# Optimization experiments

Measured on AMD Instinct MI355X. Metric: run time of the kernel, lower is better.

## Reference

```python
import jax, jax.numpy as jnp
import numpy as np

C = 0.01      # ball curvature
SC = 0.1      # sqrt(c)
K = 20        # neighbors
EPS = 1e-15


def _norm(v):
    return jnp.sqrt(jnp.clip(jnp.sum(v * v, -1, keepdims=True), EPS))


def expmap0(u):
    n = _norm(u)
    return jnp.tanh(SC * n) * u / (SC * n)


def logmap0(x):
    n = _norm(x)
    t = jnp.clip(SC * n, 0.0, 1.0 - 1e-7)
    return jnp.arctanh(t) * x / (SC * n)


def mobius_add(x, y):
    x2 = jnp.sum(x * x, -1, keepdims=True)
    y2 = jnp.sum(y * y, -1, keepdims=True)
    xy = jnp.sum(x * y, -1, keepdims=True)
    num = (1 + 2 * C * xy + C * y2) * x + (1 - C * x2) * y
    den = 1 + 2 * C * xy + C * C * x2 * y2
    return num / jnp.clip(den, EPS)


def knn(x, k):
    # x: (B,N,C) -> (B,N,k) indices of nearest neighbors (largest -dist^2)
    xx = jnp.sum(x * x, -1)                                 # (B,N)
    pd = 2.0 * jnp.einsum('bnc,bmc->bnm', x, x) - xx[:, :, None] - xx[:, None, :]
    return jax.lax.top_k(pd, k)[1]


def gather(x, idx):
    # x: (B,N,C), idx: (B,N,k) -> (B,N,k,C)
    return jax.vmap(lambda xt, ix: xt[ix])(x, idx)


def batchnorm(y, g, b, axes):
    mu = jnp.mean(y, axes)
    var = jnp.var(y, axes)
    return (y - mu) / jnp.sqrt(var + 1e-5) * g + b


def edge_block(x, w, g, b):
    # x: (B,N,C) -> (B,N,Cout); 1x1 conv over concat(nbr - ctr, ctr)
    idx = knn(x, K)
    nb = gather(x, idx)                                     # (B,N,K,C)
    ctr = jnp.broadcast_to(x[:, :, None, :], nb.shape)
    f = jnp.concatenate([nb - ctr, ctr], -1)                # (B,N,K,2C)
    y = jnp.einsum('bnkc,oc->bnko', f, w)
    y = jax.nn.leaky_relu(batchnorm(y, g, b, (0, 1, 2)), 0.2)
    return jnp.max(y, axis=2)


def setup_inputs():
    key = jax.random.key(0)
    ks = jax.random.split(key, 6)
    B, N = 8, 1024
    return {
        'x': jax.random.normal(ks[0], (B, 3, N), jnp.float32),
        'W1': jax.random.normal(ks[1], (64, 6), jnp.float32) * 0.1,
        'w2': jax.random.normal(ks[2], (64, 128), jnp.float32) * 0.05,
        'g2': jnp.ones((64,), jnp.float32), 'b2': jnp.zeros((64,), jnp.float32),
        'w3': jax.random.normal(ks[3], (128, 128), jnp.float32) * 0.05,
        'g3': jnp.ones((128,), jnp.float32), 'b3': jnp.zeros((128,), jnp.float32),
        'w4': jax.random.normal(ks[4], (256, 256), jnp.float32) * 0.05,
        'g4': jnp.ones((256,), jnp.float32), 'b4': jnp.zeros((256,), jnp.float32),
        'w5': jax.random.normal(ks[5], (1024, 512), jnp.float32) * 0.05,
        'g5': jnp.ones((1024,), jnp.float32), 'b5': jnp.zeros((1024,), jnp.float32),
    }


def reference(x, W1, w2, g2, b2, w3, g3, b3, w4, g4, b4, w5, g5, b5):
    xt = jnp.transpose(x, (0, 2, 1))                        # (B,N,3)
    # --- hyperbolic edge features ---
    idx = knn(xt, K)                                        # knn in euclidean coords
    xp = expmap0(xt)                                        # ToPoincare
    nb = gather(xp, idx)                                    # (B,N,K,3)
    ctr = jnp.broadcast_to(xp[:, :, None, :], nb.shape)
    h = jnp.concatenate([mobius_add(nb, -ctr), ctr], -1)    # (B,N,K,6)
    # MobiusConv2d (kernel 1) == mobius matvec: expmap0(W @ logmap0(x))
    h = expmap0(logmap0(h) @ W1.T)                          # (B,N,K,64)
    # MobiusBatchNorm2d (tangent-space normalization, bias=False)
    u = logmap0(h)
    mu = jnp.mean(u, axis=(0, 1, 2))
    uc = u - mu
    var = jnp.mean(jnp.sum(uc * uc, -1))
    h = expmap0(uc / jnp.sqrt(var + 1e-5))
    # Radial LeakyReLU in tangent space
    h = expmap0(jax.nn.leaky_relu(logmap0(h), 0.2))
    x1 = logmap0(jnp.max(h, axis=2))                        # max over k, FromPoincare -> (B,N,64)
    # --- euclidean DGCNN stack ---
    x2 = edge_block(x1, w2, g2, b2)                         # (B,N,64)
    x3 = edge_block(x2, w3, g3, b3)                         # (B,N,128)
    x4 = edge_block(x3, w4, g4, b4)                         # (B,N,256)
    feat = jnp.concatenate([x1, x2, x3, x4], -1)            # (B,N,512)
    y = jnp.einsum('bnc,oc->bno', feat, w5)                 # (B,N,1024)
    y = jax.nn.leaky_relu(batchnorm(y, g5, b5, (0, 1)), 0.2)
    return jnp.max(y, axis=1)                               # (B,1024)
```

## Files before the change

### kernel.cpp

```cpp
#include <hip/hip_runtime.h>
#include <math.h>

#define KNN 20
constexpr int B_ = 8, N_ = 1024, BN_ = B_ * N_;
constexpr int NEDGE = BN_ * KNN;

using f32x4 = __attribute__((ext_vector_type(4))) float;
using s8v = __attribute__((ext_vector_type(8))) short;
typedef unsigned long long u64;

__device__ __forceinline__ float wave_sum(float v) {
#pragma unroll
  for (int off = 32; off >= 1; off >>= 1) v += __shfl_xor(v, off, 64);
  return v;
}

__device__ __forceinline__ unsigned sortable(float f) {
  unsigned u = __float_as_uint(f);
  return u ^ ((u & 0x80000000u) ? 0xFFFFFFFFu : 0x80000000u);
}

__device__ __forceinline__ unsigned short rne_bf16(float f) {
  unsigned u = __float_as_uint(f);
  unsigned r = (u + 0x7FFFu + ((u >> 16) & 1u)) >> 16;
  return (unsigned short)r;
}

__device__ __forceinline__ u64 packkey(float v, int m) {
  return ((u64)sortable(v) << 10) | (u64)(1023 - m);
}

__device__ __forceinline__ void sort16_desc(u64 (&v)[16]) {
#pragma unroll
  for (int p = 1; p < 16; p <<= 1)
#pragma unroll
    for (int k = p; k >= 1; k >>= 1)
#pragma unroll
      for (int j = k & (p - 1); j + k < 16; j += 2 * k)
#pragma unroll
        for (int i = 0; i < k && i + j + k < 16; ++i)
          if ((i + j) / (2 * p) == (i + j + k) / (2 * p)) {
            u64 a = v[i + j], b = v[i + j + k];
            bool sw = a < b;
            v[i + j] = sw ? b : a;
            v[i + j + k] = sw ? a : b;
          }
}

__device__ __forceinline__ u64 bitonic64_desc(u64 B, int lane) {
#pragma unroll
  for (int k = 2; k <= 64; k <<= 1)
#pragma unroll
    for (int j = k >> 1; j > 0; j >>= 1) {
      u64 o = __shfl_xor(B, j, 64);
      bool up = ((lane & k) != 0);
      bool lower = ((lane & j) == 0);
      bool keepMin = (up == lower);
      bool takeOther = keepMin ? (o < B) : (o > B);
      B = takeOther ? o : B;
    }
  return B;
}

__device__ __forceinline__ void topk20_sorted(u64 (&v)[16], int lane,
                                              int* __restrict__ outp) {
  sort16_desc(v);
  u64 B = v[0];
#pragma unroll
  for (int s = 0; s < 15; ++s) v[s] = v[s + 1];
  v[15] = 0;
  B = bitonic64_desc(B, lane);
  for (int sel = 0; sel < KNN; ++sel) {
    u64 win = __shfl(B, 0, 64);
    int m = 1023 - (int)(win & 1023ull);
    if (lane == 0) outp[sel] = m;
    int origin = m & 63;
    u64 ins = __shfl(v[0], origin, 64);
    bool isorig = (lane == origin);
#pragma unroll
    for (int s = 0; s < 15; ++s) v[s] = isorig ? v[s + 1] : v[s];
    v[15] = isorig ? 0 : v[15];
    u64 Bs = __shfl_down(B, 1, 64);
    if (lane == 63) Bs = 0;
    unsigned long long ball = __ballot(Bs > ins);
    int pos = __popcll(ball);
    u64 Bup = __shfl_up(Bs, 1, 64);
    B = (lane < pos) ? Bs : (lane == pos ? ins : Bup);
  }
}

__global__ void k_prep(const float* __restrict__ x, float* __restrict__ xp) {
  int i = blockIdx.x * 256 + threadIdx.x;
  int b = i >> 10, n = i & 1023;
  float v0 = x[(b * 3 + 0) * N_ + n];
  float v1 = x[(b * 3 + 1) * N_ + n];
  float v2 = x[(b * 3 + 2) * N_ + n];
  float nsq = v0 * v0 + v1 * v1 + v2 * v2;
  float nn = sqrtf(fmaxf(nsq, 1e-15f));
  float s = tanhf(0.1f * nn) / (0.1f * nn);
  xp[i * 3 + 0] = s * v0; xp[i * 3 + 1] = s * v1; xp[i * 3 + 2] = s * v2;
}

__global__ __launch_bounds__(256) void k_knn3s(const float* __restrict__ x,
                                               int* __restrict__ idx) {
  __shared__ float4 pts4[N_];
  int t = threadIdx.x;
  int row0 = blockIdx.x * 4;
  int b = row0 >> 10;
  const float* xb = x + (size_t)b * 3 * N_;
  for (int i = t; i < N_; i += 256) {
    float px = xb[i], py = xb[N_ + i], pz = xb[2 * N_ + i];
    pts4[i] = make_float4(px, py, pz, px * px + py * py + pz * pz);
  }
  __syncthreads();
  int lane = t & 63, w = t >> 6;
  int row = row0 + w, rl = row & 1023;
  float4 c = pts4[rl];
  u64 v[16];
#pragma unroll
  for (int s = 0; s < 16; ++s) {
    int m = lane + 64 * s;
    float4 q = pts4[m];
    float dot = c.x * q.x + c.y * q.y + c.z * q.z;
    float val = 2.f * dot - c.w - q.w;
    v[s] = packkey(val, m);
  }
  topk20_sorted(v, lane, idx + (size_t)row * KNN);
}

__global__ __launch_bounds__(256) void k_topks(const float* __restrict__ pd,
                                               int* __restrict__ idx) {
  int t = threadIdx.x, lane = t & 63, w = t >> 6;
  int row = blockIdx.x * 4 + w;
  const float* rp = pd + (size_t)row * N_;
  u64 v[16];
#pragma unroll
  for (int s = 0; s < 16; ++s) v[s] = packkey(rp[lane + 64 * s], lane + 64 * s);
  topk20_sorted(v, lane, idx + (size_t)row * KNN);
}

__global__ __launch_bounds__(256) void k_hgeom(const float* __restrict__ xp,
                                               const int* __restrict__ idx,
                                               float* __restrict__ fgeo,
                                               float* __restrict__ mom) {
  int e = blockIdx.x * 256 + threadIdx.x;
  int gw = e / KNN;
  int b = gw >> 10;
  int nbr = idx[e];
  const float* pc = xp + (size_t)gw * 3;
  float c0 = pc[0], c1 = pc[1], c2 = pc[2];
  const float* pn = xp + ((size_t)(b << 10) + nbr) * 3;
  float a0 = pn[0], a1 = pn[1], a2 = pn[2];
  float x2 = a0 * a0 + a1 * a1 + a2 * a2;
  float y2 = c0 * c0 + c1 * c1 + c2 * c2;
  float xy = -(a0 * c0 + a1 * c1 + a2 * c2);
  float f1 = 1.f + 0.02f * xy + 0.01f * y2;
  float f2 = 1.f - 0.01f * x2;
  float den = 1.f + 0.02f * xy + 0.0001f * x2 * y2;
  float rden = 1.f / fmaxf(den, 1e-15f);
  float m0 = (f1 * a0 - f2 * c0) * rden;
  float m1 = (f1 * a1 - f2 * c1) * rden;
  float m2 = (f1 * a2 - f2 * c2) * rden;
  float nsq = m0 * m0 + m1 * m1 + m2 * m2 + y2;
  float nn = sqrtf(fmaxf(nsq, 1e-15f));
  float sn = 0.1f * nn;
  float tt = fminf(sn, 1.f - 1e-7f);
  float s = atanhf(tt) / sn;
  float f[6] = {s * m0, s * m1, s * m2, s * c0, s * c1, s * c2};
#pragma unroll
  for (int j = 0; j < 6; ++j) fgeo[j * NEDGE + e] = f[j];
  float mm[27];
  {
    int q = 0;
#pragma unroll
    for (int i = 0; i < 6; ++i) mm[q++] = f[i];
#pragma unroll
    for (int i = 0; i < 6; ++i)
#pragma unroll
      for (int j = i; j < 6; ++j) mm[q++] = f[i] * f[j];
  }
#pragma unroll
  for (int m = 0; m < 27; ++m) mm[m] = wave_sum(mm[m]);
  __shared__ float part[4][27];
  int lane = threadIdx.x & 63, w = threadIdx.x >> 6;
  if (lane == 0) {
#pragma unroll
    for (int m = 0; m < 27; ++m) part[w][m] = mm[m];
  }
  __syncthreads();
  int t = threadIdx.x;
  if (t < 27) {
    float v = part[0][t] + part[1][t] + part[2][t] + part[3][t];
    atomicAdd(&mom[t * 16 + (blockIdx.x & 15)], v);
  }
}

__global__ void k_hfin2(const float* __restrict__ mom,
                        const float* __restrict__ w1, float* mu64,
                        float* invv) {
  __shared__ float M[27];
  int t = threadIdx.x;
  if (t < 27) {
    float s = 0.f;
    for (int k = 0; k < 16; ++k) s += mom[t * 16 + k];
    M[t] = s * (1.f / (float)NEDGE);
  }
  __syncthreads();
  float w1r[6];
#pragma unroll
  for (int j = 0; j < 6; ++j) w1r[j] = w1[t * 6 + j];
  float mu = 0.f;
#pragma unroll
  for (int j = 0; j < 6; ++j) mu = fmaf(w1r[j], M[j], mu);
  float q = 0.f;
  {
    int off = 6;
#pragma unroll
    for (int i = 0; i < 6; ++i) {
      q = fmaf(w1r[i] * w1r[i], M[off], q); ++off;
#pragma unroll
      for (int j = i + 1; j < 6; ++j) {
        q = fmaf(2.f * w1r[i] * w1r[j], M[off], q); ++off;
      }
    }
  }
  float varc = q - mu * mu;
  float var = wave_sum(varc);
  mu64[t] = mu;
  if (t == 0) invv[0] = 1.f / sqrtf(var + 1e-5f);
}

__global__ __launch_bounds__(256) void k_hyper_x1(
    const float* __restrict__ fgeo, const float* __restrict__ w1,
    const float* __restrict__ mu64, const float* __restrict__ invv,
    float* __restrict__ x1, float* __restrict__ xx,
    unsigned short* __restrict__ fb) {
  int t = threadIdx.x, lane = t & 63, w = t >> 6;
  int gw = blockIdx.x * 4 + w;
  float w1r[6];
#pragma unroll
  for (int j = 0; j < 6; ++j) w1r[j] = w1[lane * 6 + j];
  float f[6] = {0.f, 0.f, 0.f, 0.f, 0.f, 0.f};
  if (lane < KNN) {
    int e = gw * KNN + lane;
#pragma unroll
    for (int j = 0; j < 6; ++j) f[j] = fgeo[j * NEDGE + e];
  }
  float mu = mu64[lane];
  float inv = invv[0];
  float mx = -INFINITY;
  for (int k = 0; k < KNN; ++k) {
    float u = 0.f;
#pragma unroll
    for (int j = 0; j < 6; ++j) u = fmaf(w1r[j], __shfl(f[j], k), u);
    float vv = (u - mu) * inv;
    float l = vv > 0.f ? vv : 0.2f * vv;
    float nsq = wave_sum(l * l);
    float nn = sqrtf(fmaxf(nsq, 1e-15f));
    float sn = 0.1f * nn;
    float sc = tanhf(sn) / sn;
    mx = fmaxf(mx, sc * l);
  }
  float msq = wave_sum(mx * mx);
  float mn = sqrtf(fmaxf(msq, 1e-15f));
  float sn = 0.1f * mn;
  float tt = fminf(sn, 1.f - 1e-7f);
  float val = atanhf(tt) / sn * mx;
  x1[(size_t)gw * 64 + lane] = val;
  fb[(size_t)gw * 512 + lane] = rne_bf16(val);
  float xs = wave_sum(val * val);
  if (lane == 0) xx[gw] = xs;
}

__device__ __forceinline__ void load_t68(float (&Lt)[64][68],
                                         const float* __restrict__ src,
                                         int ldr, int t) {
  int row = t >> 2, kq = (t & 3) * 16;
  const float* p = src + (size_t)row * ldr + kq;
  float4 v0 = *(const float4*)(p);
  float4 v1 = *(const float4*)(p + 4);
  float4 v2 = *(const float4*)(p + 8);
  float4 v3 = *(const float4*)(p + 12);
  Lt[kq + 0][row] = v0.x;  Lt[kq + 1][row] = v0.y;
  Lt[kq + 2][row] = v0.z;  Lt[kq + 3][row] = v0.w;
  Lt[kq + 4][row] = v1.x;  Lt[kq + 5][row] = v1.y;
  Lt[kq + 6][row] = v1.z;  Lt[kq + 7][row] = v1.w;
  Lt[kq + 8][row] = v2.x;  Lt[kq + 9][row] = v2.y;
  Lt[kq + 10][row] = v2.z; Lt[kq + 11][row] = v2.w;
  Lt[kq + 12][row] = v3.x; Lt[kq + 13][row] = v3.y;
  Lt[kq + 14][row] = v3.z; Lt[kq + 15][row] = v3.w;
}

template <int CIN>
__global__ __launch_bounds__(256) void k_pd2(const float* __restrict__ xin,
                                             const float* __restrict__ xx,
                                             float* __restrict__ pd) {
  __shared__ float At[64][68], Bt[64][68];
  int b = blockIdx.z;
  int n0 = blockIdx.x * 64, m0 = blockIdx.y * 64;
  int t = threadIdx.x;
  int tr4 = (t >> 4) * 4, tc4 = (t & 15) * 4;
  float acc[4][4] = {};
  const float* xb = xin + (size_t)b * N_ * CIN;
  for (int c0 = 0; c0 < CIN; c0 += 64) {
    if (c0) __syncthreads();
    load_t68(At, xb + (size_t)n0 * CIN + c0, CIN, t);
    load_t68(Bt, xb + (size_t)m0 * CIN + c0, CIN, t);
    __syncthreads();
#pragma unroll 4
    for (int k = 0; k < 64; ++k) {
      float4 a = *(const float4*)&At[k][tr4];
      float4 bb = *(const float4*)&Bt[k][tc4];
      float av[4] = {a.x, a.y, a.z, a.w};
      float bv[4] = {bb.x, bb.y, bb.z, bb.w};
#pragma unroll
      for (int ii = 0; ii < 4; ++ii)
#pragma unroll
        for (int jj = 0; jj < 4; ++jj) acc[ii][jj] = fmaf(av[ii], bv[jj], acc[ii][jj]);
    }
  }
  const float* xxn = xx + b * N_;
#pragma unroll
  for (int ii = 0; ii < 4; ++ii) {
    int r = n0 + tr4 + ii;
#pragma unroll
    for (int jj = 0; jj < 4; ++jj) {
      int c = m0 + tc4 + jj;
      pd[((size_t)b * N_ + r) * N_ + c] = 2.f * acc[ii][jj] - xxn[r] - xxn[c];
    }
  }
}

template <int CIN, int COUT>
__global__ __launch_bounds__(256) void k_xw2(const float* __restrict__ xin,
                                             const float* __restrict__ w,
                                             float* __restrict__ Y,
                                             float* __restrict__ Z) {
  __shared__ float At[64][68], Bt[64][68];
  int n0 = blockIdx.x * 64;
  int j0 = blockIdx.y * 64;
  float* outp; int obase, coff;
  if (j0 < COUT) { outp = Y; obase = j0; coff = 0; }
  else { outp = Z; obase = j0 - COUT; coff = CIN; }
  int t = threadIdx.x;
  int tr4 = (t >> 4) * 4, tc4 = (t & 15) * 4;
  float acc[4][4] = {};
  for (int c0 = 0; c0 < CIN; c0 += 64) {
    if (c0) __syncthreads();
    load_t68(At, xin + (size_t)n0 * CIN + c0, CIN, t);
    load_t68(Bt, w + (size_t)obase * (2 * CIN) + coff + c0, 2 * CIN, t);
    __syncthreads();
#pragma unroll 4
    for (int k = 0; k < 64; ++k) {
      float4 a = *(const float4*)&At[k][tr4];
      float4 bb = *(const float4*)&Bt[k][tc4];
      float av[4] = {a.x, a.y, a.z, a.w};
      float bv[4] = {bb.x, bb.y, bb.z, bb.w};
#pragma unroll
      for (int ii = 0; ii < 4; ++ii)
#pragma unroll
        for (int jj = 0; jj < 4; ++jj) acc[ii][jj] = fmaf(av[ii], bv[jj], acc[ii][jj]);
    }
  }
#pragma unroll
  for (int ii = 0; ii < 4; ++ii)
#pragma unroll
    for (int jj = 0; jj < 4; ++jj)
      outp[(size_t)(n0 + tr4 + ii) * COUT + obase + tc4 + jj] = acc[ii][jj];
}

template <int COUT>
__global__ __launch_bounds__(256) void k_gather2(
    const float* __restrict__ Y, const float* __restrict__ Z,
    const int* __restrict__ idx, float* gsum, float* gsq,
    float* __restrict__ xout) {
  constexpr int J = COUT / 64;
  int t = threadIdx.x, lane = t & 63, w = t >> 6;
  int bn = blockIdx.x * 4 + w;
  int b = bn >> 10;
  int myidx = 0;
  if (lane < KNN) myidx = idx[(size_t)bn * KNN + lane];
  float base[J], acc[J], acc2[J], mx[J];
#pragma unroll
  for (int j = 0; j < J; ++j) {
    int o = lane + 64 * j;
    base[j] = Z[(size_t)bn * COUT + o] - Y[(size_t)bn * COUT + o];
    acc[j] = 0.f; acc2[j] = 0.f; mx[j] = -INFINITY;
  }
  for (int k = 0; k < KNN; ++k) {
    int nbr = __shfl(myidx, k);
    const float* yr = Y + ((size_t)(b << 10) + nbr) * COUT;
#pragma unroll
    for (int j = 0; j < J; ++j) {
      float v = yr[lane + 64 * j] + base[j];
      acc[j] += v; acc2[j] += v * v; mx[j] = fmaxf(mx[j], v);
    }
  }
  int bkt = bn & 31;
#pragma unroll
  for (int j = 0; j < J; ++j) {
    atomicAdd(&gsum[bkt * 1024 + lane + 64 * j], acc[j]);
    atomicAdd(&gsq[bkt * 1024 + lane + 64 * j], acc2[j]);
    xout[(size_t)bn * COUT + lane + 64 * j] = mx[j];
  }
}

template <int COUT, bool WXX, bool WOUT>
__global__ void k_apply(float* __restrict__ xio,
                        const float* __restrict__ aArr,
                        const float* __restrict__ cArr,
                        unsigned short* __restrict__ fb, int coloff,
                        float* __restrict__ xx) {
  constexpr int J = COUT / 64;
  int t = threadIdx.x, lane = t & 63, w = t >> 6;
  int bn = blockIdx.x * 4 + w;
  float s = 0.f;
#pragma unroll
  for (int j = 0; j < J; ++j) {
    int o = lane + 64 * j;
    float v = xio[(size_t)bn * COUT + o];
    float u = aArr[o] * v + cArr[o];
    u = u > 0.f ? u : 0.2f * u;
    if (WOUT) xio[(size_t)bn * COUT + o] = u;
    fb[(size_t)bn * 512 + coloff + o] = rne_bf16(u);
    if (WXX) s = fmaf(u, u, s);
  }
  if (WXX) {
    s = wave_sum(s);
    if (lane == 0) xx[bn] = s;
  }
}

__global__ void k_bnfin(const float* gsum, const float* gsq,
                        const float* __restrict__ g, const float* __restrict__ bb,
                        float* aArr, float* cArr, int COUT, float Minv) {
  int ch = blockIdx.x * 256 + threadIdx.x;
  if (ch >= COUT) return;
  float S = 0, S2 = 0;
  for (int k = 0; k < 32; ++k) { S += gsum[k * 1024 + ch]; S2 += gsq[k * 1024 + ch]; }
  float mu = S * Minv;
  float var = S2 * Minv - mu * mu;
  float a = g[ch] / sqrtf(var + 1e-5f);
  aArr[ch] = a;
  cArr[ch] = bb[ch] - mu * a;
}

__global__ void k_cvt(const float* __restrict__ src,
                      unsigned short* __restrict__ dst) {
  int e = (blockIdx.x * 256 + threadIdx.x) * 4;
  float4 v = *(const float4*)(src + e);
  ushort4 o;
  o.x = rne_bf16(v.x); o.y = rne_bf16(v.y); o.z = rne_bf16(v.z); o.w = rne_bf16(v.w);
  *(ushort4*)(dst + e) = o;
}

__global__ __launch_bounds__(256) void k_fgemm3(
    const unsigned short* __restrict__ fb, const unsigned short* __restrict__ wb,
    float* gsum, float* gsq, float* __restrict__ pmax) {
  __shared__ unsigned short Bs[64][264];
  int t = threadIdx.x, lane = t & 63, w = t >> 6;
  int m0 = blockIdx.x * 128;
  int j0 = blockIdx.y * 64;
  int r16 = lane & 15, kg = lane >> 4;
  f32x4 acc[2][4];
#pragma unroll
  for (int mi = 0; mi < 2; ++mi)
#pragma unroll
    for (int nj = 0; nj < 4; ++nj) acc[mi][nj] = {0.f, 0.f, 0.f, 0.f};
  const unsigned short* pa0 = fb + (size_t)(m0 + w * 32 + r16) * 512 + kg * 8;
  const unsigned short* pa1 = pa0 + 16 * 512;
  s8v a0 = *(const s8v*)pa0;
  s8v a1 = *(const s8v*)pa1;
  int kglob = 0;
  for (int kh = 0; kh < 2; ++kh) {
    if (kh) __syncthreads();
#pragma unroll
    for (int it = 0; it < 8; ++it) {
      int chunk = it * 256 + t;
      int row = chunk >> 5;
      int kc = (chunk & 31) * 8;
      *(s8v*)&Bs[row][kc] =
          *(const s8v*)(wb + (size_t)(j0 + row) * 512 + kh * 256 + kc);
    }
    __syncthreads();
#pragma unroll
    for (int ki = 0; ki < 8; ++ki) {
      s8v na0 = a0, na1 = a1;
      int knext = kglob + 32;
      if (knext < 512) {
        na0 = *(const s8v*)(pa0 + knext);
        na1 = *(const s8v*)(pa1 + knext);
      }
      int kl = ki * 32 + kg * 8;
      s8v b0 = *(const s8v*)&Bs[r16][kl];
      s8v b1 = *(const s8v*)&Bs[r16 + 16][kl];
      s8v b2 = *(const s8v*)&Bs[r16 + 32][kl];
      s8v b3 = *(const s8v*)&Bs[r16 + 48][kl];
      acc[0][0] = __builtin_amdgcn_mfma_f32_16x16x32_bf16(a0, b0, acc[0][0], 0, 0, 0);
      acc[0][1] = __builtin_amdgcn_mfma_f32_16x16x32_bf16(a0, b1, acc[0][1], 0, 0, 0);
      acc[0][2] = __builtin_amdgcn_mfma_f32_16x16x32_bf16(a0, b2, acc[0][2], 0, 0, 0);
      acc[0][3] = __builtin_amdgcn_mfma_f32_16x16x32_bf16(a0, b3, acc[0][3], 0, 0, 0);
      acc[1][0] = __builtin_amdgcn_mfma_f32_16x16x32_bf16(a1, b0, acc[1][0], 0, 0, 0);
      acc[1][1] = __builtin_amdgcn_mfma_f32_16x16x32_bf16(a1, b1, acc[1][1], 0, 0, 0);
      acc[1][2] = __builtin_amdgcn_mfma_f32_16x16x32_bf16(a1, b2, acc[1][2], 0, 0, 0);
      acc[1][3] = __builtin_amdgcn_mfma_f32_16x16x32_bf16(a1, b3, acc[1][3], 0, 0, 0);
      a0 = na0; a1 = na1; kglob = knext;
    }
  }
  float s[4], s2[4], mx[4];
#pragma unroll
  for (int nj = 0; nj < 4; ++nj) {
    s[nj] = 0.f; s2[nj] = 0.f; mx[nj] = -INFINITY;
#pragma unroll
    for (int mi = 0; mi < 2; ++mi)
#pragma unroll
      for (int r = 0; r < 4; ++r) {
        float v = acc[mi][nj][r];
        s[nj] += v; s2[nj] += v * v; mx[nj] = fmaxf(mx[nj], v);
      }
    s[nj] += __shfl_xor(s[nj], 16, 64);  s[nj] += __shfl_xor(s[nj], 32, 64);
    s2[nj] += __shfl_xor(s2[nj], 16, 64); s2[nj] += __shfl_xor(s2[nj], 32, 64);
    mx[nj] = fmaxf(mx[nj], __shfl_xor(mx[nj], 16, 64));
    mx[nj] = fmaxf(mx[nj], __shfl_xor(mx[nj], 32, 64));
  }
  __shared__ float wsum[4][64], wsq[4][64], wmax[4][64];
  if (lane < 16) {
#pragma unroll
    for (int nj = 0; nj < 4; ++nj) {
      wsum[w][nj * 16 + lane] = s[nj];
      wsq[w][nj * 16 + lane] = s2[nj];
      wmax[w][nj * 16 + lane] = mx[nj];
    }
  }
  __syncthreads();
  if (t < 64) {
    float S = 0.f, S2 = 0.f, MX = -INFINITY;
#pragma unroll
    for (int ww = 0; ww < 4; ++ww) {
      S += wsum[ww][t]; S2 += wsq[ww][t]; MX = fmaxf(MX, wmax[ww][t]);
    }
    int o = j0 + t;
    int bkt = blockIdx.x & 31;
    atomicAdd(&gsum[bkt * 1024 + o], S);
    atomicAdd(&gsq[bkt * 1024 + o], S2);
    pmax[(size_t)(blockIdx.x & 7) * 8192 + (blockIdx.x >> 3) * 1024 + o] = MX;
  }
}

__global__ void k_fmax2(const float* __restrict__ pmax,
                        const float* __restrict__ aArr,
                        const float* __restrict__ cArr, float* __restrict__ out) {
  int j = blockIdx.x * 256 + threadIdx.x;
  int o = j & 1023;
  float mx = -INFINITY;
#pragma unroll
  for (int c = 0; c < 8; ++c) mx = fmaxf(mx, pmax[c * 8192 + j]);
  float v = aArr[o] * mx + cArr[o];
  v = v > 0.f ? v : 0.2f * v;
  out[j] = v;
}

extern "C" void kernel_launch(void* const* d_in, const int* in_sizes, int n_in,
                              void* d_out, int out_size, void* d_ws,
                              size_t ws_size, hipStream_t stream) {
  const float* x  = (const float*)d_in[0];
  const float* w1 = (const float*)d_in[1];
  const float* w2 = (const float*)d_in[2];
  const float* g2 = (const float*)d_in[3];
  const float* b2 = (const float*)d_in[4];
  const float* w3 = (const float*)d_in[5];
  const float* g3 = (const float*)d_in[6];
  const float* b3 = (const float*)d_in[7];
  const float* w4 = (const float*)d_in[8];
  const float* g4 = (const float*)d_in[9];
  const float* b4 = (const float*)d_in[10];
  const float* w5 = (const float*)d_in[11];
  const float* g5 = (const float*)d_in[12];
  const float* b5 = (const float*)d_in[13];

  float* W = (float*)d_ws;
  float* xp = W + 24576;
  float* xx = W + 49152;
  float* stats = W + 57344;
  float* aArr = stats + 262144;
  float* cArr = stats + 263168;
  float* mu64 = stats + 264192;
  float* invv = stats + 264256;
  float* mom  = stats + 264320;
  float* x1 = W + 323584;
  float* x2 = W + 847872;
  float* x3 = W + 1372160;
  float* x4 = W + 2420736;
  float* pd = W + 4517888;
  float* Y  = pd;
  float* Z  = pd + 2097152;
  float* fgeo = pd;
  int* idx = (int*)(W + 12906496);
  unsigned short* featb = (unsigned short*)(W + 13070336);
  unsigned short* w5b = (unsigned short*)(W + 13070336 + 2097152);
  float* pmax = x3;
  float* out = (float*)d_out;

  const float MinvE = 1.f / (float)(BN_ * KNN);
  float* gs0 = stats;           float* gq0 = stats + 32768;
  float* gs1 = stats + 65536;   float* gq1 = stats + 98304;
  float* gs2 = stats + 131072;  float* gq2 = stats + 163840;
  float* gs3 = stats + 196608;  float* gq3 = stats + 229376;

  hipMemsetAsync(stats, 0, 264832 * sizeof(float), stream);

  k_prep<<<32, 256, 0, stream>>>(x, xp);
  k_knn3s<<<2048, 256, 0, stream>>>(x, idx);
  k_hgeom<<<640, 256, 0, stream>>>(xp, idx, fgeo, mom);
  k_hfin2<<<1, 64, 0, stream>>>(mom, w1, mu64, invv);
  k_hyper_x1<<<2048, 256, 0, stream>>>(fgeo, w1, mu64, invv, x1, xx, featb);

  k_pd2<64><<<dim3(16, 16, 8), 256, 0, stream>>>(x1, xx, pd);
  k_topks<<<2048, 256, 0, stream>>>(pd, idx);
  k_xw2<64, 64><<<dim3(128, 2), 256, 0, stream>>>(x1, w2, Y, Z);
  k_gather2<64><<<2048, 256, 0, stream>>>(Y, Z, idx, gs0, gq0, x2);
  k_bnfin<<<1, 256, 0, stream>>>(gs0, gq0, g2, b2, aArr, cArr, 64, MinvE);
  k_apply<64, true, true><<<2048, 256, 0, stream>>>(x2, aArr, cArr, featb, 64, xx);

  k_pd2<64><<<dim3(16, 16, 8), 256, 0, stream>>>(x2, xx, pd);
  k_topks<<<2048, 256, 0, stream>>>(pd, idx);
  k_xw2<64, 128><<<dim3(128, 4), 256, 0, stream>>>(x2, w3, Y, Z);
  k_gather2<128><<<2048, 256, 0, stream>>>(Y, Z, idx, gs1, gq1, x3);
  k_bnfin<<<1, 256, 0, stream>>>(gs1, gq1, g3, b3, aArr, cArr, 128, MinvE);
  k_apply<128, true, true><<<2048, 256, 0, stream>>>(x3, aArr, cArr, featb, 128, xx);

  k_pd2<128><<<dim3(16, 16, 8), 256, 0, stream>>>(x3, xx, pd);
  k_topks<<<2048, 256, 0, stream>>>(pd, idx);
  k_xw2<128, 256><<<dim3(128, 8), 256, 0, stream>>>(x3, w4, Y, Z);
  k_gather2<256><<<2048, 256, 0, stream>>>(Y, Z, idx, gs2, gq2, x4);
  k_bnfin<<<1, 256, 0, stream>>>(gs2, gq2, g4, b4, aArr, cArr, 256, MinvE);
  k_apply<256, false, false><<<2048, 256, 0, stream>>>(x4, aArr, cArr, featb, 256, xx);

  k_cvt<<<512, 256, 0, stream>>>(w5, w5b);

  k_fgemm3<<<dim3(64, 16), 256, 0, stream>>>(featb, w5b, gs3, gq3, pmax);
  k_bnfin<<<4, 256, 0, stream>>>(gs3, gq3, g5, b5, aArr, cArr, 1024, 1.f / (float)BN_);
  k_fmax2<<<32, 256, 0, stream>>>(pmax, aArr, cArr, out);
}
```

Before: 442.1 us.

## Exploit pairwise-distance symmetry and fold w5 conversion into prep kernel

The pairwise distance kernel now computes only upper-triangular 64x64 tiles (136 per batch instead of 256). Each off-diagonal tile is transposed through shared memory and written to the mirrored location, which roughly halves the GEMM work. Separately, the w5 bf16 conversion is merged into the prep kernel, removing one launch. The trade-offs are an extra shared-memory transpose and two barriers per off-diagonal tile, a small loop to map the linear block index to a triangle position, and fewer blocks to fill the GPU.

```diff
diff --git a/kernel.cpp b/kernel.cpp
--- a/kernel.cpp
+++ b/kernel.cpp
@@ -89,16 +89,27 @@
   }
 }
 
-__global__ void k_prep(const float* __restrict__ x, float* __restrict__ xp) {
-  int i = blockIdx.x * 256 + threadIdx.x;
-  int b = i >> 10, n = i & 1023;
-  float v0 = x[(b * 3 + 0) * N_ + n];
-  float v1 = x[(b * 3 + 1) * N_ + n];
-  float v2 = x[(b * 3 + 2) * N_ + n];
-  float nsq = v0 * v0 + v1 * v1 + v2 * v2;
-  float nn = sqrtf(fmaxf(nsq, 1e-15f));
-  float s = tanhf(0.1f * nn) / (0.1f * nn);
-  xp[i * 3 + 0] = s * v0; xp[i * 3 + 1] = s * v1; xp[i * 3 + 2] = s * v2;
+__global__ void k_prep2(const float* __restrict__ x, float* __restrict__ xp,
+                        const float* __restrict__ w5,
+                        unsigned short* __restrict__ w5b) {
+  int bid = blockIdx.x;
+  if (bid < 32) {
+    int i = bid * 256 + threadIdx.x;
+    int b = i >> 10, n = i & 1023;
+    float v0 = x[(b * 3 + 0) * N_ + n];
+    float v1 = x[(b * 3 + 1) * N_ + n];
+    float v2 = x[(b * 3 + 2) * N_ + n];
+    float nsq = v0 * v0 + v1 * v1 + v2 * v2;
+    float nn = sqrtf(fmaxf(nsq, 1e-15f));
+    float s = tanhf(0.1f * nn) / (0.1f * nn);
+    xp[i * 3 + 0] = s * v0; xp[i * 3 + 1] = s * v1; xp[i * 3 + 2] = s * v2;
+  } else {
+    int e = ((bid - 32) * 256 + threadIdx.x) * 4;
+    float4 v = *(const float4*)(w5 + e);
+    ushort4 o;
+    o.x = rne_bf16(v.x); o.y = rne_bf16(v.y); o.z = rne_bf16(v.z); o.w = rne_bf16(v.w);
+    *(ushort4*)(w5b + e) = o;
+  }
 }
 
 __global__ __launch_bounds__(256) void k_knn3s(const float* __restrict__ x,
@@ -292,12 +303,16 @@
 }
 
 template <int CIN>
-__global__ __launch_bounds__(256) void k_pd2(const float* __restrict__ xin,
-                                             const float* __restrict__ xx,
-                                             float* __restrict__ pd) {
+__global__ __launch_bounds__(256) void k_pdsym(const float* __restrict__ xin,
+                                               const float* __restrict__ xx,
+                                               float* __restrict__ pd) {
   __shared__ float At[64][68], Bt[64][68];
   int b = blockIdx.z;
-  int n0 = blockIdx.x * 64, m0 = blockIdx.y * 64;
+  int id = blockIdx.x;
+  int i = 0, rem = id;
+  while (rem >= 16 - i) { rem -= 16 - i; ++i; }
+  int j = i + rem;
+  int n0 = i << 6, m0 = j << 6;
   int t = threadIdx.x;
   int tr4 = (t >> 4) * 4, tc4 = (t & 15) * 4;
   float acc[4][4] = {};
@@ -320,13 +335,28 @@
     }
   }
   const float* xxn = xx + b * N_;
+  float v[4][4];
 #pragma unroll
   for (int ii = 0; ii < 4; ++ii) {
     int r = n0 + tr4 + ii;
 #pragma unroll
     for (int jj = 0; jj < 4; ++jj) {
       int c = m0 + tc4 + jj;
-      pd[((size_t)b * N_ + r) * N_ + c] = 2.f * acc[ii][jj] - xxn[r] - xxn[c];
+      v[ii][jj] = 2.f * acc[ii][jj] - xxn[r] - xxn[c];
+      pd[((size_t)b * N_ + r) * N_ + c] = v[ii][jj];
+    }
+  }
+  if (i != j) {
+    __syncthreads();
+#pragma unroll
+    for (int ii = 0; ii < 4; ++ii)
+#pragma unroll
+      for (int jj = 0; jj < 4; ++jj) At[tc4 + jj][tr4 + ii] = v[ii][jj];
+    __syncthreads();
+#pragma unroll
+    for (int ii = 0; ii < 4; ++ii) {
+      float4 rv = *(const float4*)&At[tr4 + ii][tc4];
+      *(float4*)&pd[((size_t)b * N_ + m0 + tr4 + ii) * N_ + n0 + tc4] = rv;
     }
   }
 }
@@ -445,15 +475,6 @@
   cArr[ch] = bb[ch] - mu * a;
 }
 
-__global__ void k_cvt(const float* __restrict__ src,
-                      unsigned short* __restrict__ dst) {
-  int e = (blockIdx.x * 256 + threadIdx.x) * 4;
-  float4 v = *(const float4*)(src + e);
-  ushort4 o;
-  o.x = rne_bf16(v.x); o.y = rne_bf16(v.y); o.z = rne_bf16(v.z); o.w = rne_bf16(v.w);
-  *(ushort4*)(dst + e) = o;
-}
-
 __global__ __launch_bounds__(256) void k_fgemm3(
     const unsigned short* __restrict__ fb, const unsigned short* __restrict__ wb,
     float* gsum, float* gsq, float* __restrict__ pmax) {
@@ -609,35 +630,33 @@
 
   hipMemsetAsync(stats, 0, 264832 * sizeof(float), stream);
 
-  k_prep<<<32, 256, 0, stream>>>(x, xp);
+  k_prep2<<<32 + 512, 256, 0, stream>>>(x, xp, w5, w5b);
   k_knn3s<<<2048, 256, 0, stream>>>(x, idx);
   k_hgeom<<<640, 256, 0, stream>>>(xp, idx, fgeo, mom);
   k_hfin2<<<1, 64, 0, stream>>>(mom, w1, mu64, invv);
   k_hyper_x1<<<2048, 256, 0, stream>>>(fgeo, w1, mu64, invv, x1, xx, featb);
 
-  k_pd2<64><<<dim3(16, 16, 8), 256, 0, stream>>>(x1, xx, pd);
+  k_pdsym<64><<<dim3(136, 1, 8), 256, 0, stream>>>(x1, xx, pd);
   k_topks<<<2048, 256, 0, stream>>>(pd, idx);
   k_xw2<64, 64><<<dim3(128, 2), 256, 0, stream>>>(x1, w2, Y, Z);
   k_gather2<64><<<2048, 256, 0, stream>>>(Y, Z, idx, gs0, gq0, x2);
   k_bnfin<<<1, 256, 0, stream>>>(gs0, gq0, g2, b2, aArr, cArr, 64, MinvE);
   k_apply<64, true, true><<<2048, 256, 0, stream>>>(x2, aArr, cArr, featb, 64, xx);
 
-  k_pd2<64><<<dim3(16, 16, 8), 256, 0, stream>>>(x2, xx, pd);
+  k_pdsym<64><<<dim3(136, 1, 8), 256, 0, stream>>>(x2, xx, pd);
   k_topks<<<2048, 256, 0, stream>>>(pd, idx);
   k_xw2<64, 128><<<dim3(128, 4), 256, 0, stream>>>(x2, w3, Y, Z);
   k_gather2<128><<<2048, 256, 0, stream>>>(Y, Z, idx, gs1, gq1, x3);
   k_bnfin<<<1, 256, 0, stream>>>(gs1, gq1, g3, b3, aArr, cArr, 128, MinvE);
   k_apply<128, true, true><<<2048, 256, 0, stream>>>(x3, aArr, cArr, featb, 128, xx);
 
-  k_pd2<128><<<dim3(16, 16, 8), 256, 0, stream>>>(x3, xx, pd);
+  k_pdsym<128><<<dim3(136, 1, 8), 256, 0, stream>>>(x3, xx, pd);
   k_topks<<<2048, 256, 0, stream>>>(pd, idx);
   k_xw2<128, 256><<<dim3(128, 8), 256, 0, stream>>>(x3, w4, Y, Z);
   k_gather2<256><<<2048, 256, 0, stream>>>(Y, Z, idx, gs2, gq2, x4);
   k_bnfin<<<1, 256, 0, stream>>>(gs2, gq2, g4, b4, aArr, cArr, 256, MinvE);
   k_apply<256, false, false><<<2048, 256, 0, stream>>>(x4, aArr, cArr, featb, 256, xx);
 
-  k_cvt<<<512, 256, 0, stream>>>(w5, w5b);
-
   k_fgemm3<<<dim3(64, 16), 256, 0, stream>>>(featb, w5b, gs3, gq3, pmax);
   k_bnfin<<<4, 256, 0, stream>>>(gs3, gq3, g5, b5, aArr, cArr, 1024, 1.f / (float)BN_);
   k_fmax2<<<32, 256, 0, stream>>>(pmax, aArr, cArr, out);
```

After: 427.7 us. 1.03x faster.
